# Kernel optimization log

Measured on AMD Instinct MI355X. Metric: run time of the kernel, lower is better.

## Reference

```python
import jax, jax.numpy as jnp
import numpy as np

B, T, C = 4, 2048, 1024
WIN = 16


def setup_inputs() -> dict:
    key = jax.random.key(0)
    ks = jax.random.split(key, 5)
    s = 1.0 / np.sqrt(C)
    return {
        "x": jax.random.normal(ks[0], (B, T, C), dtype=jnp.float32),
        "Wq": jax.random.normal(ks[1], (C, C), dtype=jnp.float32) * s,
        "bq": jnp.zeros((C,), jnp.float32),
        "Wk": jax.random.normal(ks[2], (C, C), dtype=jnp.float32) * s,
        "bk": jnp.zeros((C,), jnp.float32),
        "Wv": jax.random.normal(ks[3], (C, C), dtype=jnp.float32) * s,
        "bv": jnp.zeros((C,), jnp.float32),
        "Wo": jax.random.normal(ks[4], (C, C), dtype=jnp.float32) * s,
        "bo": jnp.zeros((C,), jnp.float32),
        "window": WIN,
    }


def reference(x, Wq, bq, Wk, bk, Wv, bv, Wo, bo, window):
    Bn, Tn, Cn = x.shape
    half = window // 2
    W = 2 * half + 1  # keys per query (window [t-half, t+half])
    q = x @ Wq.T + bq
    k = x @ Wk.T + bk
    v = x @ Wv.T + bv
    offs = jnp.arange(-half, half + 1)              # [W]
    tpos = jnp.arange(Tn)                            # [T]
    idx = tpos[:, None] + offs[None, :]              # [T, W]
    valid = (idx >= 0) & (idx < Tn)                  # [T, W]
    idx_c = jnp.clip(idx, 0, Tn - 1)
    k_win = k[:, idx_c, :]                           # [B, T, W, C]
    v_win = v[:, idx_c, :]                           # [B, T, W, C]
    scale = 1.0 / jnp.sqrt(jnp.asarray(Cn, x.dtype))
    scores = jnp.einsum('btc,btwc->btw', q, k_win) * scale
    scores = jnp.where(valid[None, :, :], scores, jnp.finfo(x.dtype).min)
    attn = jax.nn.softmax(scores, axis=-1)           # [B, T, W]
    ctx = jnp.einsum('btw,btwc->btc', attn, v_win)   # [B, T, C]
    return ctx @ Wo.T + bo
```

## Files before the change

### kernel.cpp

```cpp
#include <hip/hip_runtime.h>
#include <cstdint>
#include <cstddef>

#define B_ 4
#define T_ 2048
#define C_ 1024
#define M_ (B_ * T_)
#define HALF_ 8
#define W_ 17
#define QKV_STRIDE 3072

typedef unsigned short u16;
typedef _Float16 half8 __attribute__((ext_vector_type(8)));
typedef _Float16 half2_t __attribute__((ext_vector_type(2)));
typedef float f32x16 __attribute__((ext_vector_type(16)));

__device__ __forceinline__ float dot16(half8 a, half8 b, float acc) {
#if __has_builtin(__builtin_amdgcn_fdot2)
    const half2_t* pa = (const half2_t*)&a;
    const half2_t* pb = (const half2_t*)&b;
#pragma unroll
    for (int e = 0; e < 4; ++e) acc = __builtin_amdgcn_fdot2(pa[e], pb[e], acc, false);
#else
#pragma unroll
    for (int e = 0; e < 8; ++e) acc += (float)a[e] * (float)b[e];
#endif
    return acc;
}

__global__ void prologue(const float* __restrict__ x,
                         const float* __restrict__ Wq, const float* __restrict__ Wk,
                         const float* __restrict__ Wv, const float* __restrict__ Wo,
                         const float* __restrict__ bq, const float* __restrict__ bk,
                         const float* __restrict__ bv,
                         u16* __restrict__ xh, u16* __restrict__ wcat,
                         u16* __restrict__ woh, float* __restrict__ bcat) {
    const int blk = blockIdx.x;
    if (blk >= 12288) {
        int i = (blk - 12288) * 256 + threadIdx.x;
        const float* src = (i < 1024) ? bq : (i < 2048) ? bk : bv;
        bcat[i] = src[i & 1023];
        return;
    }
    const float* src;
    u16* dst;
    int j;
    if (blk < 8192)       { src = x;  dst = xh;   j = blk * 256 + threadIdx.x; }
    else if (blk < 11264) {
        int bb = blk - 8192;
        int sel = bb >> 10;
        src = (sel == 0) ? Wq : (sel == 1) ? Wk : Wv;
        dst = wcat + ((size_t)sel << 20);
        j = (bb - (sel << 10)) * 256 + threadIdx.x;
    } else                { src = Wo; dst = woh;  j = (blk - 11264) * 256 + threadIdx.x; }
    float4 v = ((const float4*)src)[j];
    ushort4 o;
    _Float16 a = (_Float16)v.x; o.x = __builtin_bit_cast(unsigned short, a);
    _Float16 b = (_Float16)v.y; o.y = __builtin_bit_cast(unsigned short, b);
    _Float16 c = (_Float16)v.z; o.z = __builtin_bit_cast(unsigned short, c);
    _Float16 d = (_Float16)v.w; o.w = __builtin_bit_cast(unsigned short, d);
    ((ushort4*)dst)[j] = o;
}

__global__ __launch_bounds__(256) void gemm_nt_pipe(
    const u16* __restrict__ A, const u16* __restrict__ Bw,
    const float* __restrict__ bias, u16* __restrict__ Cout,
    int Ndim, int Kdim)
{
    __shared__ __align__(16) u16 As[128 * 32];
    __shared__ __align__(16) u16 Bs[128 * 32];

    const int tid  = threadIdx.x;
    const int lane = tid & 63;
    const int wave = tid >> 6;
    const int m0 = blockIdx.y * 128;
    const int n0 = blockIdx.x * 128;
    const int wm = (wave >> 1) * 64;
    const int wn = (wave & 1) * 64;

    const int srow = wave * 32 + (lane >> 2);
    const int kc = ((lane & 3) ^ ((lane >> 3) & 3)) * 8;
    const u16* Ap = A  + (size_t)(m0 + srow) * Kdim + kc;
    const u16* Bp = Bw + (size_t)(n0 + srow) * Kdim + kc;
    const size_t skip16 = (size_t)16 * Kdim;
    u16* AsL = As + wave * 1024 + lane * 8;
    u16* BsL = Bs + wave * 1024 + lane * 8;

    f32x16 acc[2][2];
#pragma unroll
    for (int i = 0; i < 2; ++i)
#pragma unroll
        for (int j = 0; j < 2; ++j)
#pragma unroll
            for (int r = 0; r < 16; ++r) acc[i][j][r] = 0.f;

    const int rr = lane & 31;
    const int hi = lane >> 5;
    const int sw = (lane >> 1) & 3;

    uint4 pa0 = *(const uint4*)(Ap);
    uint4 pa1 = *(const uint4*)(Ap + skip16);
    uint4 pb0 = *(const uint4*)(Bp);
    uint4 pb1 = *(const uint4*)(Bp + skip16);

    for (int k0 = 0; k0 < Kdim; k0 += 32) {
        if (k0) __syncthreads();
        *(uint4*)(AsL)       = pa0;
        *(uint4*)(AsL + 512) = pa1;
        *(uint4*)(BsL)       = pb0;
        *(uint4*)(BsL + 512) = pb1;
        __syncthreads();

        if (k0 + 32 < Kdim) {
            pa0 = *(const uint4*)(Ap + k0 + 32);
            pa1 = *(const uint4*)(Ap + k0 + 32 + skip16);
            pb0 = *(const uint4*)(Bp + k0 + 32);
            pb1 = *(const uint4*)(Bp + k0 + 32 + skip16);
        }

#pragma unroll
        for (int kk = 0; kk < 2; ++kk) {
            const int slot = ((kk * 2 + hi) ^ sw) * 8;
            half8 af[2], bf[2];
#pragma unroll
            for (int i = 0; i < 2; ++i)
                af[i] = *(const half8*)&As[(wm + i * 32 + rr) * 32 + slot];
#pragma unroll
            for (int j = 0; j < 2; ++j)
                bf[j] = *(const half8*)&Bs[(wn + j * 32 + rr) * 32 + slot];
#pragma unroll
            for (int i = 0; i < 2; ++i)
#pragma unroll
                for (int j = 0; j < 2; ++j)
                    acc[i][j] = __builtin_amdgcn_mfma_f32_32x32x16_f16(af[i], bf[j], acc[i][j], 0, 0, 0);
        }
    }

#pragma unroll
    for (int i = 0; i < 2; ++i) {
#pragma unroll
        for (int j = 0; j < 2; ++j) {
            const int col = n0 + wn + j * 32 + (lane & 31);
            const float bv = bias[col];
#pragma unroll
            for (int reg = 0; reg < 16; ++reg) {
                const int row = m0 + wm + i * 32 + (reg & 3) + 8 * (reg >> 2) + 4 * (lane >> 5);
                _Float16 h = (_Float16)(acc[i][j][reg] + bv);
                Cout[(size_t)row * Ndim + col] = __builtin_bit_cast(unsigned short, h);
            }
        }
    }
}

__global__ __launch_bounds__(256) void gemm_nt_64_pipe(
    const u16* __restrict__ A, const u16* __restrict__ Bw,
    const float* __restrict__ bias, float* __restrict__ Cout,
    int Ndim, int Kdim)
{
    __shared__ __align__(16) u16 As[128 * 32];
    __shared__ __align__(16) u16 Bs[64 * 32];

    const int tid  = threadIdx.x;
    const int lane = tid & 63;
    const int wave = tid >> 6;
    const int m0 = blockIdx.y * 128;
    const int n0 = blockIdx.x * 64;
    const int wm = (wave >> 1) * 64;
    const int wn = (wave & 1) * 32;

    const int sArow = wave * 32 + (lane >> 2);
    const int sBrow = wave * 16 + (lane >> 2);
    const int kc = ((lane & 3) ^ ((lane >> 3) & 3)) * 8;
    const u16* Ap = A  + (size_t)(m0 + sArow) * Kdim + kc;
    const u16* Bp = Bw + (size_t)(n0 + sBrow) * Kdim + kc;
    const size_t skip16 = (size_t)16 * Kdim;
    u16* AsL = As + wave * 1024 + lane * 8;
    u16* BsL = Bs + wave * 512  + lane * 8;

    f32x16 acc[2];
#pragma unroll
    for (int i = 0; i < 2; ++i)
#pragma unroll
        for (int r = 0; r < 16; ++r) acc[i][r] = 0.f;

    const int rr = lane & 31;
    const int hi = lane >> 5;
    const int sw = (lane >> 1) & 3;

    uint4 pa0 = *(const uint4*)(Ap);
    uint4 pa1 = *(const uint4*)(Ap + skip16);
    uint4 pb0 = *(const uint4*)(Bp);

    for (int k0 = 0; k0 < Kdim; k0 += 32) {
        if (k0) __syncthreads();
        *(uint4*)(AsL)       = pa0;
        *(uint4*)(AsL + 512) = pa1;
        *(uint4*)(BsL)       = pb0;
        __syncthreads();

        if (k0 + 32 < Kdim) {
            pa0 = *(const uint4*)(Ap + k0 + 32);
            pa1 = *(const uint4*)(Ap + k0 + 32 + skip16);
            pb0 = *(const uint4*)(Bp + k0 + 32);
        }

#pragma unroll
        for (int kk = 0; kk < 2; ++kk) {
            const int slot = ((kk * 2 + hi) ^ sw) * 8;
            half8 bf = *(const half8*)&Bs[(wn + rr) * 32 + slot];
#pragma unroll
            for (int i = 0; i < 2; ++i) {
                half8 af = *(const half8*)&As[(wm + i * 32 + rr) * 32 + slot];
                acc[i] = __builtin_amdgcn_mfma_f32_32x32x16_f16(af, bf, acc[i], 0, 0, 0);
            }
        }
    }

    const int col = n0 + wn + (lane & 31);
    const float bv = bias[col];
#pragma unroll
    for (int i = 0; i < 2; ++i) {
#pragma unroll
        for (int reg = 0; reg < 16; ++reg) {
            const int row = m0 + wm + i * 32 + (reg & 3) + 8 * (reg >> 2) + 4 * (lane >> 5);
            Cout[(size_t)row * Ndim + col] = acc[i][reg] + bv;
        }
    }
}

__global__ __launch_bounds__(256) void attn_local(
    const u16* __restrict__ qkv, u16* __restrict__ ctx)
{
    const int wid  = blockIdx.x * 4 + (threadIdx.x >> 6);
    const int lane = threadIdx.x & 63;
    const int b = wid >> 11;
    const int t = wid & (T_ - 1);
    const int base = b * T_;
    const size_t qrow = (size_t)(base + t) * QKV_STRIDE;
    const int c0 = lane * 8;

    half8 q0 = *(const half8*)(qkv + qrow + c0);
    half8 q1 = *(const half8*)(qkv + qrow + 512 + c0);

    float s[W_];
#pragma unroll
    for (int o = 0; o < W_; ++o) {
        int j = t - HALF_ + o;
        int jc = min(max(j, 0), T_ - 1);
        const size_t kb = (size_t)(base + jc) * QKV_STRIDE + 1024;
        half8 k0v = *(const half8*)(qkv + kb + c0);
        half8 k1v = *(const half8*)(qkv + kb + 512 + c0);
        float d = dot16(q1, k1v, dot16(q0, k0v, 0.f));
#pragma unroll
        for (int off = 32; off > 0; off >>= 1)
            d += __shfl_xor(d, off);
        s[o] = (j == jc) ? d * 0.03125f : -3.0e38f;
    }

    float mx = s[0];
#pragma unroll
    for (int o = 1; o < W_; ++o) mx = fmaxf(mx, s[o]);
    float den = 0.f;
#pragma unroll
    for (int o = 0; o < W_; ++o) den += __expf(s[o] - mx);
    const float inv = 1.f / den;

    float acc0[8], acc1[8];
#pragma unroll
    for (int e = 0; e < 8; ++e) { acc0[e] = 0.f; acc1[e] = 0.f; }
#pragma unroll
    for (int o = 0; o < W_; ++o) {
        int j = t - HALF_ + o;
        int jc = min(max(j, 0), T_ - 1);
        const float wt = __expf(s[o] - mx) * inv;
        const size_t vb_ = (size_t)(base + jc) * QKV_STRIDE + 2048;
        half8 v0 = *(const half8*)(qkv + vb_ + c0);
        half8 v1 = *(const half8*)(qkv + vb_ + 512 + c0);
#pragma unroll
        for (int e = 0; e < 8; ++e) {
            acc0[e] += wt * (float)v0[e];
            acc1[e] += wt * (float)v1[e];
        }
    }

    const size_t crow = (size_t)(base + t) * C_;
    half8 o0, o1;
#pragma unroll
    for (int e = 0; e < 8; ++e) { o0[e] = (_Float16)acc0[e]; o1[e] = (_Float16)acc1[e]; }
    *(half8*)(ctx + crow + c0) = o0;
    *(half8*)(ctx + crow + 512 + c0) = o1;
}

extern "C" void kernel_launch(void* const* d_in, const int* in_sizes, int n_in,
                              void* d_out, int out_size, void* d_ws, size_t ws_size,
                              hipStream_t stream) {
    const float* x  = (const float*)d_in[0];
    const float* Wq = (const float*)d_in[1];
    const float* bq = (const float*)d_in[2];
    const float* Wk = (const float*)d_in[3];
    const float* bk = (const float*)d_in[4];
    const float* Wv = (const float*)d_in[5];
    const float* bv = (const float*)d_in[6];
    const float* Wo = (const float*)d_in[7];
    const float* bo = (const float*)d_in[8];
    float* out = (float*)d_out;

    u16* xh   = (u16*)d_ws;
    u16* wcat = xh   + (size_t)M_ * C_;
    u16* woh  = wcat + (size_t)3 * C_ * C_;
    u16* qkvh = woh  + (size_t)C_ * C_;
    u16* ctxh = qkvh + (size_t)M_ * QKV_STRIDE;
    float* bcat = (float*)(ctxh + (size_t)M_ * C_);

    prologue<<<12300, 256, 0, stream>>>(x, Wq, Wk, Wv, Wo, bq, bk, bv,
                                        xh, wcat, woh, bcat);

    dim3 gqkv(QKV_STRIDE / 128, M_ / 128);
    gemm_nt_pipe<<<gqkv, 256, 0, stream>>>(xh, wcat, bcat, qkvh, QKV_STRIDE, C_);

    attn_local<<<M_ / 4, 256, 0, stream>>>(qkvh, ctxh);

    dim3 go(C_ / 64, M_ / 128);
    gemm_nt_64_pipe<<<go, 256, 0, stream>>>(ctxh, woh, bo, out, C_, C_);
}
```

Baseline: 238.7 us.

## Pre-pack weights into MFMA fragment layout and load B directly from global

Weight matrices are now converted to fp16 in a fragment-major layout that matches the MFMA B-operand register pattern, done by a new conversion kernel. The GEMM kernels then read B fragments straight from global memory into registers with coalesced 16-byte loads, dropping the B shared-memory tile, its stores and its LDS reads. This cuts LDS traffic and shared-memory footprint. In exchange, the B loads are issued at the top of each k-step with little prefetch distance, so global latency may be exposed, and each wave re-reads its B fragments from L2 instead of sharing them through LDS.

```diff
diff --git a/kernel.cpp b/kernel.cpp
--- a/kernel.cpp
+++ b/kernel.cpp
@@ -28,47 +28,63 @@
     return acc;
 }
 
-__global__ void prologue(const float* __restrict__ x,
-                         const float* __restrict__ Wq, const float* __restrict__ Wk,
-                         const float* __restrict__ Wv, const float* __restrict__ Wo,
-                         const float* __restrict__ bq, const float* __restrict__ bk,
-                         const float* __restrict__ bv,
-                         u16* __restrict__ xh, u16* __restrict__ wcat,
-                         u16* __restrict__ woh, float* __restrict__ bcat) {
-    const int blk = blockIdx.x;
-    if (blk >= 12288) {
-        int i = (blk - 12288) * 256 + threadIdx.x;
-        const float* src = (i < 1024) ? bq : (i < 2048) ? bk : bv;
-        bcat[i] = src[i & 1023];
-        return;
-    }
-    const float* src;
-    u16* dst;
-    int j;
-    if (blk < 8192)       { src = x;  dst = xh;   j = blk * 256 + threadIdx.x; }
-    else if (blk < 11264) {
-        int bb = blk - 8192;
-        int sel = bb >> 10;
-        src = (sel == 0) ? Wq : (sel == 1) ? Wk : Wv;
-        dst = wcat + ((size_t)sel << 20);
-        j = (bb - (sel << 10)) * 256 + threadIdx.x;
-    } else                { src = Wo; dst = woh;  j = (blk - 11264) * 256 + threadIdx.x; }
-    float4 v = ((const float4*)src)[j];
+__device__ __forceinline__ ushort4 cvt4(float4 v) {
     ushort4 o;
     _Float16 a = (_Float16)v.x; o.x = __builtin_bit_cast(unsigned short, a);
     _Float16 b = (_Float16)v.y; o.y = __builtin_bit_cast(unsigned short, b);
     _Float16 c = (_Float16)v.z; o.z = __builtin_bit_cast(unsigned short, c);
     _Float16 d = (_Float16)v.w; o.w = __builtin_bit_cast(unsigned short, d);
-    ((ushort4*)dst)[j] = o;
-}
-
-__global__ __launch_bounds__(256) void gemm_nt_pipe(
-    const u16* __restrict__ A, const u16* __restrict__ Bw,
+    return o;
+}
+
+__global__ void prologue(const float* __restrict__ x,
+                         const float* __restrict__ bq, const float* __restrict__ bk,
+                         const float* __restrict__ bv,
+                         u16* __restrict__ xh, float* __restrict__ bcat) {
+    const int blk = blockIdx.x;
+    if (blk >= 8192) {
+        int i = (blk - 8192) * 256 + threadIdx.x;
+        const float* src = (i < 1024) ? bq : (i < 2048) ? bk : bv;
+        bcat[i] = src[i & 1023];
+        return;
+    }
+    int j = blk * 256 + threadIdx.x;
+    ((ushort4*)xh)[j] = cvt4(((const float4*)x)[j]);
+}
+
+__global__ void wfrag(const float* __restrict__ Wq, const float* __restrict__ Wk,
+                      const float* __restrict__ Wv, const float* __restrict__ Wo,
+                      u16* __restrict__ wfq, u16* __restrict__ wfo) {
+    int c = blockIdx.x * 256 + threadIdx.x;
+    const float* src;
+    u16* dst;
+    int cc;
+    if (c < 393216) {
+        int mat = c / 131072;
+        src = (mat == 0) ? Wq : (mat == 1) ? Wk : Wv;
+        dst = wfq;  cc = c;  c = c % 131072;
+    } else {
+        src = Wo;  dst = wfo;  cc = c - 393216;  c = cc;
+    }
+    const int nt_local = c >> 12;
+    const int ks   = (c >> 6) & 63;
+    const int lane = c & 63;
+    const int row = nt_local * 32 + (lane & 31);
+    const int col = ks * 16 + (lane >> 5) * 8;
+    const float4* s = (const float4*)(src + (size_t)row * C_ + col);
+    ushort4 lo = cvt4(s[0]);
+    ushort4 hi = cvt4(s[1]);
+    ushort4* d = (ushort4*)(dst + (size_t)cc * 8);
+    d[0] = lo;
+    d[1] = hi;
+}
+
+__global__ __launch_bounds__(256) void gemm_nt_bfrag(
+    const u16* __restrict__ A, const u16* __restrict__ Bfrag,
     const float* __restrict__ bias, u16* __restrict__ Cout,
     int Ndim, int Kdim)
 {
     __shared__ __align__(16) u16 As[128 * 32];
-    __shared__ __align__(16) u16 Bs[128 * 32];
 
     const int tid  = threadIdx.x;
     const int lane = tid & 63;
@@ -76,15 +92,17 @@
     const int m0 = blockIdx.y * 128;
     const int n0 = blockIdx.x * 128;
     const int wm = (wave >> 1) * 64;
-    const int wn = (wave & 1) * 64;
+    const int wnt = blockIdx.x * 4 + (wave & 1) * 2;
 
     const int srow = wave * 32 + (lane >> 2);
     const int kc = ((lane & 3) ^ ((lane >> 3) & 3)) * 8;
-    const u16* Ap = A  + (size_t)(m0 + srow) * Kdim + kc;
-    const u16* Bp = Bw + (size_t)(n0 + srow) * Kdim + kc;
+    const u16* Ap = A + (size_t)(m0 + srow) * Kdim + kc;
     const size_t skip16 = (size_t)16 * Kdim;
     u16* AsL = As + wave * 1024 + lane * 8;
-    u16* BsL = Bs + wave * 1024 + lane * 8;
+
+    const int nks = Kdim >> 4;
+    const u16* Bf0 = Bfrag + ((size_t)(wnt + 0) * nks) * 512 + lane * 8;
+    const u16* Bf1 = Bfrag + ((size_t)(wnt + 1) * nks) * 512 + lane * 8;
 
     f32x16 acc[2][2];
 #pragma unroll
@@ -100,39 +118,37 @@
 
     uint4 pa0 = *(const uint4*)(Ap);
     uint4 pa1 = *(const uint4*)(Ap + skip16);
-    uint4 pb0 = *(const uint4*)(Bp);
-    uint4 pb1 = *(const uint4*)(Bp + skip16);
 
     for (int k0 = 0; k0 < Kdim; k0 += 32) {
+        const int ks = k0 >> 4;
+        half8 bfr[2][2];
+        bfr[0][0] = *(const half8*)(Bf0 + (size_t)ks * 512);
+        bfr[0][1] = *(const half8*)(Bf1 + (size_t)ks * 512);
+        bfr[1][0] = *(const half8*)(Bf0 + (size_t)(ks + 1) * 512);
+        bfr[1][1] = *(const half8*)(Bf1 + (size_t)(ks + 1) * 512);
+
         if (k0) __syncthreads();
         *(uint4*)(AsL)       = pa0;
         *(uint4*)(AsL + 512) = pa1;
-        *(uint4*)(BsL)       = pb0;
-        *(uint4*)(BsL + 512) = pb1;
         __syncthreads();
 
         if (k0 + 32 < Kdim) {
             pa0 = *(const uint4*)(Ap + k0 + 32);
             pa1 = *(const uint4*)(Ap + k0 + 32 + skip16);
-            pb0 = *(const uint4*)(Bp + k0 + 32);
-            pb1 = *(const uint4*)(Bp + k0 + 32 + skip16);
         }
 
 #pragma unroll
         for (int kk = 0; kk < 2; ++kk) {
             const int slot = ((kk * 2 + hi) ^ sw) * 8;
-            half8 af[2], bf[2];
+            half8 af[2];
 #pragma unroll
             for (int i = 0; i < 2; ++i)
                 af[i] = *(const half8*)&As[(wm + i * 32 + rr) * 32 + slot];
 #pragma unroll
-            for (int j = 0; j < 2; ++j)
-                bf[j] = *(const half8*)&Bs[(wn + j * 32 + rr) * 32 + slot];
-#pragma unroll
             for (int i = 0; i < 2; ++i)
 #pragma unroll
                 for (int j = 0; j < 2; ++j)
-                    acc[i][j] = __builtin_amdgcn_mfma_f32_32x32x16_f16(af[i], bf[j], acc[i][j], 0, 0, 0);
+                    acc[i][j] = __builtin_amdgcn_mfma_f32_32x32x16_f16(af[i], bfr[kk][j], acc[i][j], 0, 0, 0);
         }
     }
 
@@ -140,7 +156,7 @@
     for (int i = 0; i < 2; ++i) {
 #pragma unroll
         for (int j = 0; j < 2; ++j) {
-            const int col = n0 + wn + j * 32 + (lane & 31);
+            const int col = (wnt + j) * 32 + (lane & 31);
             const float bv = bias[col];
 #pragma unroll
             for (int reg = 0; reg < 16; ++reg) {
@@ -152,30 +168,28 @@
     }
 }
 
-__global__ __launch_bounds__(256) void gemm_nt_64_pipe(
-    const u16* __restrict__ A, const u16* __restrict__ Bw,
+__global__ __launch_bounds__(256) void gemm_nt_64_bfrag(
+    const u16* __restrict__ A, const u16* __restrict__ Bfrag,
     const float* __restrict__ bias, float* __restrict__ Cout,
     int Ndim, int Kdim)
 {
     __shared__ __align__(16) u16 As[128 * 32];
-    __shared__ __align__(16) u16 Bs[64 * 32];
 
     const int tid  = threadIdx.x;
     const int lane = tid & 63;
     const int wave = tid >> 6;
     const int m0 = blockIdx.y * 128;
-    const int n0 = blockIdx.x * 64;
     const int wm = (wave >> 1) * 64;
-    const int wn = (wave & 1) * 32;
-
-    const int sArow = wave * 32 + (lane >> 2);
-    const int sBrow = wave * 16 + (lane >> 2);
+    const int wnt = blockIdx.x * 2 + (wave & 1);
+
+    const int srow = wave * 32 + (lane >> 2);
     const int kc = ((lane & 3) ^ ((lane >> 3) & 3)) * 8;
-    const u16* Ap = A  + (size_t)(m0 + sArow) * Kdim + kc;
-    const u16* Bp = Bw + (size_t)(n0 + sBrow) * Kdim + kc;
+    const u16* Ap = A + (size_t)(m0 + srow) * Kdim + kc;
     const size_t skip16 = (size_t)16 * Kdim;
     u16* AsL = As + wave * 1024 + lane * 8;
-    u16* BsL = Bs + wave * 512  + lane * 8;
+
+    const int nks = Kdim >> 4;
+    const u16* Bf = Bfrag + ((size_t)wnt * nks) * 512 + lane * 8;
 
     f32x16 acc[2];
 #pragma unroll
@@ -189,34 +203,35 @@
 
     uint4 pa0 = *(const uint4*)(Ap);
     uint4 pa1 = *(const uint4*)(Ap + skip16);
-    uint4 pb0 = *(const uint4*)(Bp);
 
     for (int k0 = 0; k0 < Kdim; k0 += 32) {
+        const int ks = k0 >> 4;
+        half8 bfr[2];
+        bfr[0] = *(const half8*)(Bf + (size_t)ks * 512);
+        bfr[1] = *(const half8*)(Bf + (size_t)(ks + 1) * 512);
+
         if (k0) __syncthreads();
         *(uint4*)(AsL)       = pa0;
         *(uint4*)(AsL + 512) = pa1;
-        *(uint4*)(BsL)       = pb0;
         __syncthreads();
 
         if (k0 + 32 < Kdim) {
             pa0 = *(const uint4*)(Ap + k0 + 32);
             pa1 = *(const uint4*)(Ap + k0 + 32 + skip16);
-            pb0 = *(const uint4*)(Bp + k0 + 32);
         }
 
 #pragma unroll
         for (int kk = 0; kk < 2; ++kk) {
             const int slot = ((kk * 2 + hi) ^ sw) * 8;
-            half8 bf = *(const half8*)&Bs[(wn + rr) * 32 + slot];
 #pragma unroll
             for (int i = 0; i < 2; ++i) {
                 half8 af = *(const half8*)&As[(wm + i * 32 + rr) * 32 + slot];
-                acc[i] = __builtin_amdgcn_mfma_f32_32x32x16_f16(af, bf, acc[i], 0, 0, 0);
+                acc[i] = __builtin_amdgcn_mfma_f32_32x32x16_f16(af, bfr[kk], acc[i], 0, 0, 0);
             }
         }
     }
 
-    const int col = n0 + wn + (lane & 31);
+    const int col = wnt * 32 + (lane & 31);
     const float bv = bias[col];
 #pragma unroll
     for (int i = 0; i < 2; ++i) {
@@ -306,20 +321,20 @@
     float* out = (float*)d_out;
 
     u16* xh   = (u16*)d_ws;
-    u16* wcat = xh   + (size_t)M_ * C_;
-    u16* woh  = wcat + (size_t)3 * C_ * C_;
-    u16* qkvh = woh  + (size_t)C_ * C_;
+    u16* wfq  = xh   + (size_t)M_ * C_;
+    u16* wfo  = wfq  + (size_t)3 * C_ * C_;
+    u16* qkvh = wfo  + (size_t)C_ * C_;
     u16* ctxh = qkvh + (size_t)M_ * QKV_STRIDE;
     float* bcat = (float*)(ctxh + (size_t)M_ * C_);
 
-    prologue<<<12300, 256, 0, stream>>>(x, Wq, Wk, Wv, Wo, bq, bk, bv,
-                                        xh, wcat, woh, bcat);
+    prologue<<<8204, 256, 0, stream>>>(x, bq, bk, bv, xh, bcat);
+    wfrag<<<2048, 256, 0, stream>>>(Wq, Wk, Wv, Wo, wfq, wfo);
 
     dim3 gqkv(QKV_STRIDE / 128, M_ / 128);
-    gemm_nt_pipe<<<gqkv, 256, 0, stream>>>(xh, wcat, bcat, qkvh, QKV_STRIDE, C_);
+    gemm_nt_bfrag<<<gqkv, 256, 0, stream>>>(xh, wfq, bcat, qkvh, QKV_STRIDE, C_);
 
     attn_local<<<M_ / 4, 256, 0, stream>>>(qkvh, ctxh);
 
     dim3 go(C_ / 64, M_ / 128);
-    gemm_nt_64_pipe<<<go, 256, 0, stream>>>(ctxh, woh, bo, out, C_, C_);
-}
+    gemm_nt_64_bfrag<<<go, 256, 0, stream>>>(ctxh, wfo, bo, out, C_, C_);
+}
```

Result: no change. 240.3 us (+0.7%).
